# Performance work log

Hardware: AMD Instinct MI355X
Metric: run time of the kernel (lower is better)

The kernel has to match this reference:

```python
import jax, jax.numpy as jnp
import numpy as np

# SofthebbArgs constants (rate, adaptive=True, p, dot_uw=False, temp)
RATE = 1e-3
TEMP = 1.0
P = 0.5


def negate_non_maximal(t):
    # keep the per-row max entry, negate all others
    idx = jnp.argmax(t, axis=-1)                      # [B]
    mask = idx[:, None] == jnp.arange(t.shape[-1])    # [B, OUT]
    return jnp.where(mask, t, -t)


def setup_inputs() -> dict:
    key = jax.random.key(0)
    k1, k2 = jax.random.split(key, 2)
    B, IN, OUT = 8192, 1024, 1024
    x = jax.random.normal(k1, (B, IN), dtype=jnp.float32)
    # xavier_normal_ with gain=1: std = sqrt(2/(fan_in+fan_out))
    W = jax.random.normal(k2, (OUT, IN), dtype=jnp.float32) * (2.0 / (IN + OUT)) ** 0.5
    b = jnp.zeros((OUT,), dtype=jnp.float32)
    return {"x": x, "W": W, "b": b}


def reference(x, W, b):
    # --- HebbianLinear.forward (act = Identity) ---
    u = x @ W.T + b                                   # [B, OUT]
    y = u
    # --- softhebb: y = softmax(y / temp), then _hebb with dot_uw=False ---
    ysm = jax.nn.softmax(y / TEMP, axis=1)
    yn = negate_non_maximal(ysm)                      # [B, OUT]
    Bn = x.shape[0]
    # _hebb materializes dw[b,o,i] = yn[b,o]*(x[b,i] - u[b,o]*W[o,i]) then means over b.
    # Algebraically fused (no [B,OUT,IN] intermediate):
    #   step[o,i] = (yn^T x)[o,i]/B - mean_b(yn[b,o]*u[b,o]) * W[o,i]
    step = (yn.T @ x) / Bn - jnp.mean(yn * u, axis=0)[:, None] * W  # [OUT, IN]
    # adaptive per-row rate: rate * |1 - ||W_row||_2|^p
    diff = jnp.abs(1.0 - jnp.linalg.norm(W, axis=1))  # [OUT]
    rate = RATE * diff ** P
    return rate[:, None] * step                       # [OUT, IN]
```

## Files before the change

kernel.cpp:

```cpp
#include <hip/hip_runtime.h>

#define BATCH 8192
#define INF_  1024
#define OUTF  1024
#define INV_B (1.0f/8192.0f)
#define RATE_C 1e-3f
#define SPLITZ 8

typedef __bf16 bf16x8 __attribute__((ext_vector_type(8)));
typedef float  f32x4  __attribute__((ext_vector_type(4)));
typedef const __attribute__((address_space(1))) unsigned int* gas_t;
typedef __attribute__((address_space(3))) unsigned int* las_t;

static __device__ __forceinline__ unsigned short f2bf(float f) {
  unsigned int u = __float_as_uint(f);
  u += 0x7fffu + ((u >> 16) & 1u);
  return (unsigned short)(u >> 16);
}

__global__ __launch_bounds__(256) void k_convert_x(
    const float* __restrict__ x, unsigned short* __restrict__ xb,
    unsigned short* __restrict__ xT) {
  __shared__ unsigned short tl[64][72];
  const int t  = threadIdx.x;
  const int r0 = blockIdx.y * 64;
  const int c0 = blockIdx.x * 64;
  const int rr = t >> 4;
  const int cc = (t & 15) * 4;
#pragma unroll
  for (int p = 0; p < 4; ++p) {
    int r = p * 16 + rr;
    float4 v = *(const float4*)&x[(size_t)(r0 + r) * INF_ + c0 + cc];
    ushort4 h;
    h.x = f2bf(v.x); h.y = f2bf(v.y); h.z = f2bf(v.z); h.w = f2bf(v.w);
    *(ushort4*)&xb[(size_t)(r0 + r) * INF_ + c0 + cc] = h;
    tl[cc + 0][r] = h.x; tl[cc + 1][r] = h.y;
    tl[cc + 2][r] = h.z; tl[cc + 3][r] = h.w;
  }
  __syncthreads();
#pragma unroll
  for (int p = 0; p < 4; ++p) {
    int c = p * 16 + rr;
    ushort4 w = *(const ushort4*)&tl[c][cc];
    *(ushort4*)&xT[(size_t)(c0 + c) * BATCH + r0 + cc] = w;
  }
}

__global__ __launch_bounds__(256) void k_convert_w(
    const float* __restrict__ W, unsigned short* __restrict__ Wb,
    float* __restrict__ rate) {
  __shared__ float red[256];
  const int t = threadIdx.x;
  const int o = blockIdx.x;
  float4 v = *(const float4*)&W[(size_t)o * INF_ + t * 4];
  ushort4 h;
  h.x = f2bf(v.x); h.y = f2bf(v.y); h.z = f2bf(v.z); h.w = f2bf(v.w);
  *(ushort4*)&Wb[(size_t)o * INF_ + t * 4] = h;
  red[t] = v.x * v.x + v.y * v.y + v.z * v.z + v.w * v.w;
  __syncthreads();
  for (int s = 128; s > 0; s >>= 1) {
    if (t < s) red[t] += red[t + s];
    __syncthreads();
  }
  if (t == 0) {
    float nrm = sqrtf(red[0]);
    rate[o] = RATE_C * sqrtf(fabsf(1.0f - nrm));
  }
}

__global__ __launch_bounds__(256, 2) void k_gemm(
    const unsigned short* __restrict__ A, const unsigned short* __restrict__ B,
    int lda, int ldb, int kChunk, float* __restrict__ C, int ldc,
    const float* __restrict__ bias, int mode) {
  __shared__ unsigned short As[128 * 64];
  __shared__ unsigned short Bs[128 * 64];
  const int t    = threadIdx.x;
  const int m0   = blockIdx.y * 128;
  const int n0   = blockIdx.x * 128;
  const int k0   = blockIdx.z * kChunk;
  const int lane = t & 63;
  const int wave = t >> 6;
  const int sr   = lane >> 3;
  const int scx  = ((lane & 7) ^ sr) * 8;
  const int wm   = (wave >> 1) * 64;
  const int wn   = (wave & 1) * 64;
  const int fm   = lane & 15;
  const int fk   = (lane >> 4) * 8;

  f32x4 acc[4][4] = {};

  const int ldsRow0 = wave * 8;
  const size_t gArow = (size_t)(m0 + ldsRow0 + sr) * lda + scx;
  const size_t gBrow = (size_t)(n0 + ldsRow0 + sr) * ldb + scx;

  for (int ks = 0; ks < kChunk; ks += 64) {
    const int k = k0 + ks;
#pragma unroll
    for (int j = 0; j < 4; ++j) {
      __builtin_amdgcn_global_load_lds(
          (gas_t)&A[gArow + (size_t)j * 32 * lda + k],
          (las_t)&As[(ldsRow0 + j * 32) * 64], 16, 0, 0);
      __builtin_amdgcn_global_load_lds(
          (gas_t)&B[gBrow + (size_t)j * 32 * ldb + k],
          (las_t)&Bs[(ldsRow0 + j * 32) * 64], 16, 0, 0);
    }
    __syncthreads();
#pragma unroll
    for (int kk = 0; kk < 64; kk += 32) {
      bf16x8 af[4], bf[4];
      const int swz = ((((kk + fk) >> 3) ^ (fm & 7)) << 3);
#pragma unroll
      for (int i = 0; i < 4; ++i)
        af[i] = *(const bf16x8*)&As[(wm + i * 16 + fm) * 64 + swz];
#pragma unroll
      for (int i = 0; i < 4; ++i)
        bf[i] = *(const bf16x8*)&Bs[(wn + i * 16 + fm) * 64 + swz];
#pragma unroll
      for (int mt = 0; mt < 4; ++mt)
#pragma unroll
        for (int nt = 0; nt < 4; ++nt)
          acc[mt][nt] = __builtin_amdgcn_mfma_f32_16x16x32_bf16(
              af[mt], bf[nt], acc[mt][nt], 0, 0, 0);
    }
    __syncthreads();
  }

  const int er = (lane >> 4) * 4;
  if (mode == 0) {
#pragma unroll
    for (int nt = 0; nt < 4; ++nt) {
      const int n  = n0 + wn + nt * 16 + fm;
      const float bv = bias[n];
#pragma unroll
      for (int mt = 0; mt < 4; ++mt) {
        const int mb = m0 + wm + mt * 16 + er;
#pragma unroll
        for (int r = 0; r < 4; ++r)
          C[(size_t)(mb + r) * ldc + n] = acc[mt][nt][r] + bv;
      }
    }
  } else {
    float* Cp = C + (size_t)blockIdx.z * (1024u * 1024u);
#pragma unroll
    for (int nt = 0; nt < 4; ++nt) {
      const int n = n0 + wn + nt * 16 + fm;
#pragma unroll
      for (int mt = 0; mt < 4; ++mt) {
        const int mb = m0 + wm + mt * 16 + er;
#pragma unroll
        for (int r = 0; r < 4; ++r)
          Cp[(size_t)(mb + r) * ldc + n] = acc[mt][nt][r];
      }
    }
  }
}

__global__ __launch_bounds__(256) void k_row_stats(
    const float* __restrict__ u, const float* __restrict__ x,
    const float* __restrict__ W, float* __restrict__ rowmax,
    float* __restrict__ rowinv, int* __restrict__ rowarg) {
  __shared__ float rv[256];
  __shared__ int   ri[256];
  __shared__ int   cnt;
  __shared__ int   cands[32];
  const int t = threadIdx.x;
  const int b = blockIdx.x;
  if (t == 0) cnt = 0;
  float4 v = *(const float4*)&u[(size_t)b * OUTF + t * 4];
  float mv = v.x; int mi = t * 4;
  if (v.y > mv) { mv = v.y; mi = t * 4 + 1; }
  if (v.z > mv) { mv = v.z; mi = t * 4 + 2; }
  if (v.w > mv) { mv = v.w; mi = t * 4 + 3; }
  rv[t] = mv; ri[t] = mi;
  __syncthreads();
  for (int s = 128; s > 0; s >>= 1) {
    if (t < s) {
      if (rv[t + s] > rv[t] || (rv[t + s] == rv[t] && ri[t + s] < ri[t])) {
        rv[t] = rv[t + s]; ri[t] = ri[t + s];
      }
    }
    __syncthreads();
  }
  const float M    = rv[0];
  const int   argA = ri[0];
  __syncthreads();
  float se = __expf(v.x - M) + __expf(v.y - M) + __expf(v.z - M) + __expf(v.w - M);
  rv[t] = se;
  __syncthreads();
  for (int s = 128; s > 0; s >>= 1) {
    if (t < s) rv[t] += rv[t + s];
    __syncthreads();
  }
  const float total = rv[0];
  const float thr = M - 0.05f;
  if (v.x >= thr) { int p = atomicAdd(&cnt, 1); if (p < 32) cands[p] = t * 4; }
  if (v.y >= thr) { int p = atomicAdd(&cnt, 1); if (p < 32) cands[p] = t * 4 + 1; }
  if (v.z >= thr) { int p = atomicAdd(&cnt, 1); if (p < 32) cands[p] = t * 4 + 2; }
  if (v.w >= thr) { int p = atomicAdd(&cnt, 1); if (p < 32) cands[p] = t * 4 + 3; }
  __syncthreads();
  int nc = cnt; if (nc > 32) nc = 32;
  int best = argA;
  if (nc > 1) {
    float4 xv = *(const float4*)&x[(size_t)b * INF_ + t * 4];
    float bv = -3.4e38f; int bi = 0x7fffffff;
    for (int c = 0; c < nc; ++c) {
      const int o = cands[c];
      __syncthreads();
      float4 wv = *(const float4*)&W[(size_t)o * INF_ + t * 4];
      rv[t] = xv.x * wv.x + xv.y * wv.y + xv.z * wv.z + xv.w * wv.w;
      __syncthreads();
      for (int s = 128; s > 0; s >>= 1) {
        if (t < s) rv[t] += rv[t + s];
        __syncthreads();
      }
      const float ev = rv[0];
      if (ev > bv || (ev == bv && o < bi)) { bv = ev; bi = o; }
    }
    best = bi;
  }
  if (t == 0) {
    rowmax[b] = M;
    rowinv[b] = 1.0f / total;
    rowarg[b] = best;
  }
}

__global__ __launch_bounds__(256) void k_yn(
    const float* __restrict__ u, const float* __restrict__ rowmax,
    const float* __restrict__ rowinv, const int* __restrict__ rowarg,
    unsigned short* __restrict__ ynT, float* __restrict__ s) {
  __shared__ unsigned short tile[256][72];
  __shared__ float smax[64], sinv[64];
  __shared__ int   sarg[64];
  const int t  = threadIdx.x;
  const int o0 = blockIdx.x * 256;
  const int b0 = blockIdx.y * 64;
  if (t < 64) {
    smax[t] = rowmax[b0 + t];
    sinv[t] = rowinv[b0 + t];
    sarg[t] = rowarg[b0 + t];
  }
  __syncthreads();
  const int o = o0 + t;
  float sacc = 0.0f;
#pragma unroll 4
  for (int r = 0; r < 64; ++r) {
    float uu  = u[(size_t)(b0 + r) * OUTF + o];
    float ysm = __expf(uu - smax[r]) * sinv[r];
    float yn  = (o == sarg[r]) ? ysm : -ysm;
    sacc += yn * uu;
    tile[t][r] = f2bf(yn);
  }
  atomicAdd(&s[o], sacc);
  __syncthreads();
#pragma unroll
  for (int it = 0; it < 8; ++it) {
    const int row = it * 32 + (t >> 3);
    const int seg = (t & 7) * 8;
    uint4 vv = *(const uint4*)&tile[row][seg];
    *(uint4*)&ynT[(size_t)(o0 + row) * BATCH + b0 + seg] = vv;
  }
}

__global__ __launch_bounds__(256) void k_final(
    const float* __restrict__ Cp, const float* __restrict__ W,
    const float* __restrict__ s, const float* __restrict__ rate,
    float* __restrict__ out) {
  const int g  = blockIdx.x * 256 + threadIdx.x;
  const int i4 = g * 4;
  const int o  = i4 >> 10;
  float4 c = *(const float4*)&Cp[i4];
#pragma unroll
  for (int z = 1; z < SPLITZ; ++z) {
    float4 cz = *(const float4*)&Cp[(size_t)z * (1024u * 1024u) + i4];
    c.x += cz.x; c.y += cz.y; c.z += cz.z; c.w += cz.w;
  }
  float4 w = *(const float4*)&W[i4];
  const float sb = s[o] * INV_B;
  const float rt = rate[o];
  float4 r;
  r.x = rt * (c.x * INV_B - sb * w.x);
  r.y = rt * (c.y * INV_B - sb * w.y);
  r.z = rt * (c.z * INV_B - sb * w.z);
  r.w = rt * (c.w * INV_B - sb * w.w);
  *(float4*)&out[i4] = r;
}

extern "C" void kernel_launch(void* const* d_in, const int* in_sizes, int n_in,
                              void* d_out, int out_size, void* d_ws, size_t ws_size,
                              hipStream_t stream) {
  const float* x    = (const float*)d_in[0];
  const float* W    = (const float*)d_in[1];
  const float* bias = (const float*)d_in[2];
  float* out = (float*)d_out;
  char* ws = (char*)d_ws;

  float*          u    = (float*)(ws + 0);
  unsigned short* xb   = (unsigned short*)(ws + 33554432);
  unsigned short* xT   = (unsigned short*)(ws + 50331648);
  unsigned short* Wb   = (unsigned short*)(ws + 67108864);
  unsigned short* ynT  = (unsigned short*)(ws + 69206016);
  float*          svec = (float*)(ws + 85983232);
  float*          rate = (float*)(ws + 85987328);
  float*          rmax = (float*)(ws + 85991424);
  float*          rinv = (float*)(ws + 86024192);
  int*            rarg = (int*)  (ws + 86056960);

  hipMemsetAsync(svec, 0, OUTF * sizeof(float), stream);

  k_convert_x<<<dim3(16, 128), 256, 0, stream>>>(x, xb, xT);
  k_convert_w<<<dim3(1024), 256, 0, stream>>>(W, Wb, rate);
  k_gemm<<<dim3(8, 64, 1), 256, 0, stream>>>(xb, Wb, 1024, 1024, 1024,
                                             u, 1024, bias, 0);
  k_row_stats<<<dim3(8192), 256, 0, stream>>>(u, x, W, rmax, rinv, rarg);
  k_yn<<<dim3(4, 128), 256, 0, stream>>>(u, rmax, rinv, rarg, ynT, svec);
  k_gemm<<<dim3(8, 8, SPLITZ), 256, 0, stream>>>(ynT, xT, 8192, 8192,
                                                 8192 / SPLITZ, u, 1024,
                                                 nullptr, 1);
  k_final<<<dim3(1024), 256, 0, stream>>>(u, W, svec, rate, out);
}
```

Measured before the change: 178.4 us.

## Fuse conversion kernels, remap GEMM block order, warp-per-row stats, packed yn stores

Merges the x and W conversion kernels into one launch that also zeroes the s vector, which removes the memset and a launch. Both GEMMs use a 1D grid with a custom block-index mapping so that consecutively scheduled blocks share operand tiles in cache. Row statistics now use one wave per row with shuffle reductions in place of block-wide LDS reductions and barriers. k_yn packs eight bf16 values per vector LDS store. Each piece mainly cuts launch count, synchronisation or memory traffic, and the fused convert kernel now has divergent block roles.

```diff
diff --git a/kernel.cpp b/kernel.cpp
--- a/kernel.cpp
+++ b/kernel.cpp
@@ -18,13 +18,37 @@
   return (unsigned short)(u >> 16);
 }
 
-__global__ __launch_bounds__(256) void k_convert_x(
+__global__ __launch_bounds__(256) void k_convert(
     const float* __restrict__ x, unsigned short* __restrict__ xb,
-    unsigned short* __restrict__ xT) {
+    unsigned short* __restrict__ xT, const float* __restrict__ W,
+    unsigned short* __restrict__ Wb, float* __restrict__ rate,
+    float* __restrict__ svec) {
+  const int t = threadIdx.x;
+  if (blockIdx.x >= 2048) {
+    __shared__ float red[256];
+    const int o = blockIdx.x - 2048;
+    float4 v = *(const float4*)&W[(size_t)o * INF_ + t * 4];
+    ushort4 h;
+    h.x = f2bf(v.x); h.y = f2bf(v.y); h.z = f2bf(v.z); h.w = f2bf(v.w);
+    *(ushort4*)&Wb[(size_t)o * INF_ + t * 4] = h;
+    red[t] = v.x * v.x + v.y * v.y + v.z * v.z + v.w * v.w;
+    __syncthreads();
+    for (int s = 128; s > 0; s >>= 1) {
+      if (t < s) red[t] += red[t + s];
+      __syncthreads();
+    }
+    if (t == 0) {
+      float nrm = sqrtf(red[0]);
+      rate[o] = RATE_C * sqrtf(fabsf(1.0f - nrm));
+      svec[o] = 0.0f;
+    }
+    return;
+  }
   __shared__ unsigned short tl[64][72];
-  const int t  = threadIdx.x;
-  const int r0 = blockIdx.y * 64;
-  const int c0 = blockIdx.x * 64;
+  const int bx = blockIdx.x & 15;
+  const int by = blockIdx.x >> 4;
+  const int r0 = by * 64;
+  const int c0 = bx * 64;
   const int rr = t >> 4;
   const int cc = (t & 15) * 4;
 #pragma unroll
@@ -46,38 +70,27 @@
   }
 }
 
-__global__ __launch_bounds__(256) void k_convert_w(
-    const float* __restrict__ W, unsigned short* __restrict__ Wb,
-    float* __restrict__ rate) {
-  __shared__ float red[256];
-  const int t = threadIdx.x;
-  const int o = blockIdx.x;
-  float4 v = *(const float4*)&W[(size_t)o * INF_ + t * 4];
-  ushort4 h;
-  h.x = f2bf(v.x); h.y = f2bf(v.y); h.z = f2bf(v.z); h.w = f2bf(v.w);
-  *(ushort4*)&Wb[(size_t)o * INF_ + t * 4] = h;
-  red[t] = v.x * v.x + v.y * v.y + v.z * v.z + v.w * v.w;
-  __syncthreads();
-  for (int s = 128; s > 0; s >>= 1) {
-    if (t < s) red[t] += red[t + s];
-    __syncthreads();
-  }
-  if (t == 0) {
-    float nrm = sqrtf(red[0]);
-    rate[o] = RATE_C * sqrtf(fabsf(1.0f - nrm));
-  }
-}
-
 __global__ __launch_bounds__(256, 2) void k_gemm(
     const unsigned short* __restrict__ A, const unsigned short* __restrict__ B,
     int lda, int ldb, int kChunk, float* __restrict__ C, int ldc,
     const float* __restrict__ bias, int mode) {
   __shared__ unsigned short As[128 * 64];
   __shared__ unsigned short Bs[128 * 64];
-  const int t    = threadIdx.x;
-  const int m0   = blockIdx.y * 128;
-  const int n0   = blockIdx.x * 128;
-  const int k0   = blockIdx.z * kChunk;
+  const int t  = threadIdx.x;
+  const int id = blockIdx.x;
+  int bx, by, bz;
+  if (mode == 0) {
+    by = (id & 7) | ((id >> 6) << 3);
+    bx = (id >> 3) & 7;
+    bz = 0;
+  } else {
+    bz = id & 7;
+    by = (id >> 3) & 7;
+    bx = id >> 6;
+  }
+  const int m0   = by * 128;
+  const int n0   = bx * 128;
+  const int k0   = bz * kChunk;
   const int lane = t & 63;
   const int wave = t >> 6;
   const int sr   = lane >> 3;
@@ -140,7 +153,7 @@
       }
     }
   } else {
-    float* Cp = C + (size_t)blockIdx.z * (1024u * 1024u);
+    float* Cp = C + (size_t)bz * (1024u * 1024u);
 #pragma unroll
     for (int nt = 0; nt < 4; ++nt) {
       const int n = n0 + wn + nt * 16 + fm;
@@ -159,68 +172,81 @@
     const float* __restrict__ u, const float* __restrict__ x,
     const float* __restrict__ W, float* __restrict__ rowmax,
     float* __restrict__ rowinv, int* __restrict__ rowarg) {
-  __shared__ float rv[256];
-  __shared__ int   ri[256];
-  __shared__ int   cnt;
-  __shared__ int   cands[32];
-  const int t = threadIdx.x;
-  const int b = blockIdx.x;
-  if (t == 0) cnt = 0;
-  float4 v = *(const float4*)&u[(size_t)b * OUTF + t * 4];
-  float mv = v.x; int mi = t * 4;
-  if (v.y > mv) { mv = v.y; mi = t * 4 + 1; }
-  if (v.z > mv) { mv = v.z; mi = t * 4 + 2; }
-  if (v.w > mv) { mv = v.w; mi = t * 4 + 3; }
-  rv[t] = mv; ri[t] = mi;
-  __syncthreads();
-  for (int s = 128; s > 0; s >>= 1) {
-    if (t < s) {
-      if (rv[t + s] > rv[t] || (rv[t + s] == rv[t] && ri[t + s] < ri[t])) {
-        rv[t] = rv[t + s]; ri[t] = ri[t + s];
+  __shared__ int cands[4][32];
+  __shared__ int cnt[4];
+  const int lane = threadIdx.x & 63;
+  const int wave = threadIdx.x >> 6;
+  const int b    = blockIdx.x * 4 + wave;
+
+  float a[16];
+  const float* up = &u[(size_t)b * OUTF + lane * 16];
+#pragma unroll
+  for (int j = 0; j < 16; j += 4) {
+    float4 v = *(const float4*)&up[j];
+    a[j] = v.x; a[j + 1] = v.y; a[j + 2] = v.z; a[j + 3] = v.w;
+  }
+  float mv = a[0]; int mi = lane * 16;
+#pragma unroll
+  for (int j = 1; j < 16; ++j)
+    if (a[j] > mv) { mv = a[j]; mi = lane * 16 + j; }
+#pragma unroll
+  for (int off = 1; off < 64; off <<= 1) {
+    float ov = __shfl_xor(mv, off);
+    int   oi = __shfl_xor(mi, off);
+    if (ov > mv || (ov == mv && oi < mi)) { mv = ov; mi = oi; }
+  }
+  const float M = mv;
+  float se = 0.0f;
+#pragma unroll
+  for (int j = 0; j < 16; ++j) se += __expf(a[j] - M);
+#pragma unroll
+  for (int off = 1; off < 64; off <<= 1) se += __shfl_xor(se, off);
+
+  const float thr = M - 0.05f;
+  int ccount = 0;
+  unsigned int cflags = 0;
+#pragma unroll
+  for (int j = 0; j < 16; ++j)
+    if (a[j] >= thr) { cflags |= (1u << j); ++ccount; }
+  int tot = ccount;
+#pragma unroll
+  for (int off = 1; off < 64; off <<= 1) tot += __shfl_xor(tot, off);
+
+  int best = mi;
+  if (tot > 1) {
+    if (lane == 0) cnt[wave] = 0;
+    for (int j = 0; j < 16; ++j)
+      if (cflags & (1u << j)) {
+        int p = atomicAdd(&cnt[wave], 1);
+        if (p < 32) cands[wave][p] = lane * 16 + j;
       }
-    }
-    __syncthreads();
-  }
-  const float M    = rv[0];
-  const int   argA = ri[0];
-  __syncthreads();
-  float se = __expf(v.x - M) + __expf(v.y - M) + __expf(v.z - M) + __expf(v.w - M);
-  rv[t] = se;
-  __syncthreads();
-  for (int s = 128; s > 0; s >>= 1) {
-    if (t < s) rv[t] += rv[t + s];
-    __syncthreads();
-  }
-  const float total = rv[0];
-  const float thr = M - 0.05f;
-  if (v.x >= thr) { int p = atomicAdd(&cnt, 1); if (p < 32) cands[p] = t * 4; }
-  if (v.y >= thr) { int p = atomicAdd(&cnt, 1); if (p < 32) cands[p] = t * 4 + 1; }
-  if (v.z >= thr) { int p = atomicAdd(&cnt, 1); if (p < 32) cands[p] = t * 4 + 2; }
-  if (v.w >= thr) { int p = atomicAdd(&cnt, 1); if (p < 32) cands[p] = t * 4 + 3; }
-  __syncthreads();
-  int nc = cnt; if (nc > 32) nc = 32;
-  int best = argA;
-  if (nc > 1) {
-    float4 xv = *(const float4*)&x[(size_t)b * INF_ + t * 4];
+    int nc = cnt[wave]; if (nc > 32) nc = 32;
+    float xr[16];
+    const float* xp = &x[(size_t)b * INF_ + lane * 16];
+#pragma unroll
+    for (int j = 0; j < 16; j += 4) {
+      float4 v = *(const float4*)&xp[j];
+      xr[j] = v.x; xr[j + 1] = v.y; xr[j + 2] = v.z; xr[j + 3] = v.w;
+    }
     float bv = -3.4e38f; int bi = 0x7fffffff;
     for (int c = 0; c < nc; ++c) {
-      const int o = cands[c];
-      __syncthreads();
-      float4 wv = *(const float4*)&W[(size_t)o * INF_ + t * 4];
-      rv[t] = xv.x * wv.x + xv.y * wv.y + xv.z * wv.z + xv.w * wv.w;
-      __syncthreads();
-      for (int s = 128; s > 0; s >>= 1) {
-        if (t < s) rv[t] += rv[t + s];
-        __syncthreads();
+      const int o = cands[wave][c];
+      const float* wp = &W[(size_t)o * INF_ + lane * 16];
+      float d = 0.0f;
+#pragma unroll
+      for (int j = 0; j < 16; j += 4) {
+        float4 v = *(const float4*)&wp[j];
+        d += xr[j] * v.x + xr[j + 1] * v.y + xr[j + 2] * v.z + xr[j + 3] * v.w;
       }
-      const float ev = rv[0];
-      if (ev > bv || (ev == bv && o < bi)) { bv = ev; bi = o; }
+#pragma unroll
+      for (int off = 1; off < 64; off <<= 1) d += __shfl_xor(d, off);
+      if (d > bv || (d == bv && o < bi)) { bv = d; bi = o; }
     }
     best = bi;
   }
-  if (t == 0) {
+  if (lane == 0) {
     rowmax[b] = M;
-    rowinv[b] = 1.0f / total;
+    rowinv[b] = 1.0f / se;
     rowarg[b] = best;
   }
 }
@@ -243,13 +269,20 @@
   __syncthreads();
   const int o = o0 + t;
   float sacc = 0.0f;
-#pragma unroll 4
-  for (int r = 0; r < 64; ++r) {
-    float uu  = u[(size_t)(b0 + r) * OUTF + o];
-    float ysm = __expf(uu - smax[r]) * sinv[r];
-    float yn  = (o == sarg[r]) ? ysm : -ysm;
-    sacc += yn * uu;
-    tile[t][r] = f2bf(yn);
+#pragma unroll
+  for (int g = 0; g < 8; ++g) {
+    uint4 pkv;
+    unsigned short* pk = (unsigned short*)&pkv;
+#pragma unroll
+    for (int j = 0; j < 8; ++j) {
+      const int r = g * 8 + j;
+      float uu  = u[(size_t)(b0 + r) * OUTF + o];
+      float ysm = __expf(uu - smax[r]) * sinv[r];
+      float yn  = (o == sarg[r]) ? ysm : -ysm;
+      sacc += yn * uu;
+      pk[j] = f2bf(yn);
+    }
+    *(uint4*)&tile[t][g * 8] = pkv;
   }
   atomicAdd(&s[o], sacc);
   __syncthreads();
@@ -306,16 +339,13 @@
   float*          rinv = (float*)(ws + 86024192);
   int*            rarg = (int*)  (ws + 86056960);
 
-  hipMemsetAsync(svec, 0, OUTF * sizeof(float), stream);
-
-  k_convert_x<<<dim3(16, 128), 256, 0, stream>>>(x, xb, xT);
-  k_convert_w<<<dim3(1024), 256, 0, stream>>>(W, Wb, rate);
-  k_gemm<<<dim3(8, 64, 1), 256, 0, stream>>>(xb, Wb, 1024, 1024, 1024,
-                                             u, 1024, bias, 0);
-  k_row_stats<<<dim3(8192), 256, 0, stream>>>(u, x, W, rmax, rinv, rarg);
+  k_convert<<<dim3(3072), 256, 0, stream>>>(x, xb, xT, W, Wb, rate, svec);
+  k_gemm<<<dim3(512), 256, 0, stream>>>(xb, Wb, 1024, 1024, 1024,
+                                        u, 1024, bias, 0);
+  k_row_stats<<<dim3(2048), 256, 0, stream>>>(u, x, W, rmax, rinv, rarg);
   k_yn<<<dim3(4, 128), 256, 0, stream>>>(u, rmax, rinv, rarg, ynT, svec);
-  k_gemm<<<dim3(8, 8, SPLITZ), 256, 0, stream>>>(ynT, xT, 8192, 8192,
-                                                 8192 / SPLITZ, u, 1024,
-                                                 nullptr, 1);
+  k_gemm<<<dim3(512), 256, 0, stream>>>(ynT, xT, 8192, 8192,
+                                        8192 / SPLITZ, u, 1024,
+                                        nullptr, 1);
   k_final<<<dim3(1024), 256, 0, stream>>>(u, W, svec, rate, out);
 }
```

Result: faster. 158.8 us (-11.0%).
